# Performance work log

Hardware: AMD Instinct MI355X
Metric: run time of the kernel (lower is better)

The kernel has to match this reference:

```python
import jax, jax.numpy as jnp
import numpy as np

N_NODES = 100000
NEG_SLOPE = 0.2


def gat_conv(x, edge_src, edge_dst, W, att_src, att_dst, bias):
    """PyG-style GATConv with heads=1. edge_src/edge_dst include self-loops.
    x: [N, F_in], W: [F_in, F_out], att_src/att_dst: [F_out], bias: [F_out].
    """
    n = x.shape[0]
    h = x @ W  # [N, F_out]
    a_src = h @ att_src  # [N]
    a_dst = h @ att_dst  # [N]
    e = jax.nn.leaky_relu(a_src[edge_src] + a_dst[edge_dst], NEG_SLOPE)  # [E]
    # segment softmax over edges sharing a destination node
    m = jax.ops.segment_max(e, edge_dst, num_segments=n)  # [N]; self-loops ensure no empty segment
    p = jnp.exp(e - m[edge_dst])
    denom = jax.ops.segment_sum(p, edge_dst, num_segments=n)  # [N]
    alpha = p / denom[edge_dst]  # [E]
    out = jax.ops.segment_sum(alpha[:, None] * h[edge_src], edge_dst, num_segments=n)
    return out + bias


def setup_inputs() -> dict:
    key = jax.random.key(0)
    ks = jax.random.split(key, 16)
    n, e = N_NODES, 1_600_000
    f_in, f_hid, f_out = 128, 64, 32
    x = jax.random.normal(ks[0], (n, f_in), dtype=jnp.float32)
    edge_index = jax.random.randint(ks[1], (2, e), 0, n, dtype=jnp.int32)

    def lin(k, fi, fo):
        return jax.random.normal(k, (fi, fo), dtype=jnp.float32) / np.sqrt(fi).astype(np.float32)

    def att(k, fo):
        return jax.random.normal(k, (fo,), dtype=jnp.float32) / np.sqrt(fo).astype(np.float32)

    return {
        "x": x, "edge_index": edge_index,
        "W1": lin(ks[2], f_in, f_hid), "as1": att(ks[3], f_hid), "ad1": att(ks[4], f_hid),
        "b1": jnp.zeros((f_hid,), jnp.float32),
        "W2": lin(ks[5], f_hid, f_hid), "as2": att(ks[6], f_hid), "ad2": att(ks[7], f_hid),
        "b2": jnp.zeros((f_hid,), jnp.float32),
        "W3": lin(ks[8], f_hid, f_out), "as3": att(ks[9], f_out), "ad3": att(ks[10], f_out),
        "b3": jnp.zeros((f_out,), jnp.float32),
    }


def reference(x, edge_index, W1, as1, ad1, b1, W2, as2, ad2, b2, W3, as3, ad3, b3):
    n = x.shape[0]
    # PyG GATConv default add_self_loops=True
    loops = jnp.arange(n, dtype=edge_index.dtype)
    src = jnp.concatenate([edge_index[0], loops])
    dst = jnp.concatenate([edge_index[1], loops])

    h1 = jax.nn.relu(gat_conv(x, src, dst, W1, as1, ad1, b1))
    h2 = jax.nn.relu(gat_conv(h1, src, dst, W2, as2, ad2, b2))
    out = gat_conv(h2, src, dst, W3, as3, ad3, b3)
    return (out, h1, h2)
```

## Files before the change

### kernel.cpp

```cpp
#include <hip/hip_runtime.h>
#include <hip/hip_bf16.h>

#define NEG_SLOPE 0.2f

__device__ __forceinline__ unsigned short bf16bits(float f) {
    __hip_bfloat16 t = __float2bfloat16(f);
    return *reinterpret_cast<unsigned short*>(&t);
}

template <int FIN, int FOUT>
__global__ __launch_bounds__(256) void node_linear(
    const float* __restrict__ x, const float* __restrict__ W,
    const float* __restrict__ att_s, const float* __restrict__ att_d,
    __hip_bfloat16* __restrict__ h, float* __restrict__ a_s, float* __restrict__ a_d, int n)
{
    constexpr int FG = FOUT / 4;
    constexpr int NG = 256 / FG;
    constexpr int NB = NG * 4;
    constexpr int RS = FIN + 4;
    __shared__ float xs[NB * RS];

    const int tid = threadIdx.x;
    const int base = blockIdx.x * NB;

    constexpr int CNT = NB * FIN / 4 / 256;
    #pragma unroll
    for (int i = 0; i < CNT; ++i) {
        int f4 = tid + 256 * i;
        int node = f4 / (FIN / 4);
        int kk = f4 % (FIN / 4);
        float4 v = make_float4(0.f, 0.f, 0.f, 0.f);
        if (base + node < n) v = *(const float4*)(x + (size_t)(base + node) * FIN + kk * 4);
        *(float4*)(xs + node * RS + kk * 4) = v;
    }
    __syncthreads();

    const int fg = tid % FG;
    const int ng = tid / FG;
    const float* wp = W + fg * 4;
    const float* xr0 = xs + (ng * 4 + 0) * RS;
    const float* xr1 = xs + (ng * 4 + 1) * RS;
    const float* xr2 = xs + (ng * 4 + 2) * RS;
    const float* xr3 = xs + (ng * 4 + 3) * RS;

    float a00=0,a01=0,a02=0,a03=0, a10=0,a11=0,a12=0,a13=0;
    float a20=0,a21=0,a22=0,a23=0, a30=0,a31=0,a32=0,a33=0;
    #pragma unroll 4
    for (int k = 0; k < FIN; ++k) {
        float4 w = *(const float4*)(wp + (size_t)k * FOUT);
        float x0 = xr0[k], x1 = xr1[k], x2 = xr2[k], x3 = xr3[k];
        a00 = fmaf(x0, w.x, a00); a01 = fmaf(x0, w.y, a01);
        a02 = fmaf(x0, w.z, a02); a03 = fmaf(x0, w.w, a03);
        a10 = fmaf(x1, w.x, a10); a11 = fmaf(x1, w.y, a11);
        a12 = fmaf(x1, w.z, a12); a13 = fmaf(x1, w.w, a13);
        a20 = fmaf(x2, w.x, a20); a21 = fmaf(x2, w.y, a21);
        a22 = fmaf(x2, w.z, a22); a23 = fmaf(x2, w.w, a23);
        a30 = fmaf(x3, w.x, a30); a31 = fmaf(x3, w.y, a31);
        a32 = fmaf(x3, w.z, a32); a33 = fmaf(x3, w.w, a33);
    }

    const float4 ats = *(const float4*)(att_s + fg * 4);
    const float4 atd = *(const float4*)(att_d + fg * 4);
    float acc[4][4] = {{a00,a01,a02,a03},{a10,a11,a12,a13},
                       {a20,a21,a22,a23},{a30,a31,a32,a33}};
    #pragma unroll
    for (int i = 0; i < 4; ++i) {
        int node = base + ng * 4 + i;
        float ps = acc[i][0]*ats.x + acc[i][1]*ats.y + acc[i][2]*ats.z + acc[i][3]*ats.w;
        float pd = acc[i][0]*atd.x + acc[i][1]*atd.y + acc[i][2]*atd.z + acc[i][3]*atd.w;
        #pragma unroll
        for (int o = FG / 2; o > 0; o >>= 1) {
            ps += __shfl_xor(ps, o);
            pd += __shfl_xor(pd, o);
        }
        if (fg == 0 && node < n) { a_s[node] = ps; a_d[node] = pd; }
        if (node < n) {
            unsigned w0 = (unsigned)bf16bits(acc[i][0]) | ((unsigned)bf16bits(acc[i][1]) << 16);
            unsigned w1 = (unsigned)bf16bits(acc[i][2]) | ((unsigned)bf16bits(acc[i][3]) << 16);
            uint2 pk; pk.x = w0; pk.y = w1;
            *reinterpret_cast<uint2*>(h + (size_t)node * FOUT + fg * 4) = pk;
        }
    }
}


__global__ __launch_bounds__(256) void sb_hist(
    const int* __restrict__ edst, int E, int n, int* __restrict__ sbhist)
{
    __shared__ int lh[256];
    const int tid = threadIdx.x;
    lh[tid] = 0;
    __syncthreads();
    const int Etot = E + n;
    const int stride = gridDim.x * 256;
    for (int i = blockIdx.x * 256 + tid; i < Etot; i += stride) {
        int d = (i < E) ? edst[i] : i - E;
        atomicAdd(&lh[d >> 9], 1);
    }
    __syncthreads();
    if (lh[tid] > 0) atomicAdd(&sbhist[tid], lh[tid]);
}

__global__ __launch_bounds__(256) void sb_scan(
    const int* __restrict__ sbhist, int nsb, int Etot,
    int* __restrict__ sbbase, int* __restrict__ sbcur)
{
    __shared__ int buf[256];
    const int tid = threadIdx.x;
    int v = (tid < nsb) ? sbhist[tid] : 0;
    buf[tid] = v;
    __syncthreads();
    for (int off = 1; off < 256; off <<= 1) {
        int t = (tid >= off) ? buf[tid - off] : 0;
        __syncthreads();
        buf[tid] += t;
        __syncthreads();
    }
    if (tid < nsb) {
        int ex = buf[tid] - v;
        sbbase[tid] = ex;
        sbcur[tid] = ex;
    }
    if (tid == 0) sbbase[nsb] = Etot;
}

#define CB_CHUNK 4096
#define CB_NSB_MAX 256
__global__ __launch_bounds__(256) void chunk_bin(
    const int* __restrict__ esrc, const int* __restrict__ edst, int E, int n,
    int nsb, int* __restrict__ sbcur, int* __restrict__ packed1)
{
    __shared__ int pk[CB_CHUNK];
    __shared__ unsigned short sbv[CB_CHUNK];
    __shared__ int hist[CB_NSB_MAX];
    __shared__ int gbase[CB_NSB_MAX];
    const int tid = threadIdx.x;
    const int i0 = blockIdx.x * CB_CHUNK;
    const int Etot = E + n;

    hist[tid] = 0;
    __syncthreads();

    for (int j = tid; j < CB_CHUNK; j += 256) {
        int i = i0 + j;
        if (i < Etot) {
            int s, d;
            if (i < E) { s = esrc[i]; d = edst[i]; }
            else       { s = d = i - E; }
            int sb = d >> 9;
            pk[j] = ((d & 511) << 17) | s;
            sbv[j] = (unsigned short)sb;
            atomicAdd(&hist[sb], 1);
        } else {
            sbv[j] = 0xFFFFu;
        }
    }
    __syncthreads();

    if (tid < nsb && hist[tid] > 0)
        gbase[tid] = atomicAdd(&sbcur[tid], hist[tid]);
    hist[tid] = 0;
    __syncthreads();

    for (int j = tid; j < CB_CHUNK; j += 256) {
        unsigned short sb = sbv[j];
        if (sb != 0xFFFFu) {
            int pos = gbase[sb] + atomicAdd(&hist[sb], 1);
            packed1[pos] = pk[j];
        }
    }
}

__global__ __launch_bounds__(256) void sb_sort2(
    const int* __restrict__ sbbase, const int* __restrict__ packed1,
    int* __restrict__ col, int* __restrict__ row_end, int n)
{
    const int sb = blockIdx.x;
    const int node0 = sb << 9;
    const int lo = sbbase[sb];
    const int hi = sbbase[sb + 1];
    const int tid = threadIdx.x;
    __shared__ int c[512];
    __shared__ int sc[512];
    c[tid] = 0; c[tid + 256] = 0;
    __syncthreads();
    for (int j = lo + tid; j < hi; j += 256)
        atomicAdd(&c[((unsigned)packed1[j]) >> 17], 1);
    __syncthreads();
    sc[tid] = c[tid]; sc[tid + 256] = c[tid + 256];
    __syncthreads();
    for (int off = 1; off < 512; off <<= 1) {
        int i0 = tid, i1 = tid + 256;
        int v0 = (i0 >= off) ? sc[i0 - off] : 0;
        int v1 = (i1 >= off) ? sc[i1 - off] : 0;
        __syncthreads();
        sc[i0] += v0; sc[i1] += v1;
        __syncthreads();
    }
    #pragma unroll
    for (int q = 0; q < 2; ++q) {
        int i = tid + q * 256;
        int node = node0 + i;
        if (node < n) row_end[node] = lo + sc[i];
        c[i] = lo + sc[i] - c[i];
    }
    __syncthreads();
    for (int j = lo + tid; j < hi; j += 256) {
        int p = packed1[j];
        int ld = ((unsigned)p) >> 17;
        int pos = atomicAdd(&c[ld], 1);
        col[pos] = p & 0x1FFFF;
    }
}

template <int FOUT>
__global__ __launch_bounds__(256) void gat_aggregate(
    const int* __restrict__ row_end, const int* __restrict__ col,
    const float* __restrict__ a_s, const float* __restrict__ a_d,
    const __hip_bfloat16* __restrict__ h, const float* __restrict__ bias,
    float* __restrict__ outp, int n, int do_relu)
{
    constexpr int NPW = 64 / FOUT;
    const int gwave = (blockIdx.x * 256 + threadIdx.x) >> 6;
    const int lane = threadIdx.x & 63;
    const int node = gwave * NPW + lane / FOUT;
    const int f = lane % FOUT;
    if (node >= n) return;
    const int end = row_end[node];
    const int start = (node == 0) ? 0 : row_end[node - 1];
    const float adn = a_d[node];
    const int egrp = (FOUT == 64) ? 0 : (lane & 32);
    float acc = 0.f, den = 0.f;
    for (int j = start; j < end; j += 8) {
        int k_idx = j + (lane & 7);
        int clamped = (k_idx < end) ? k_idx : (end - 1);
        int sown = col[clamped];
        float eown = a_s[sown] + adn;
        eown = (eown > 0.f) ? eown : NEG_SLOPE * eown;
        float pown = (k_idx < end) ? __expf(eown) : 0.f;
        #pragma unroll
        for (int k = 0; k < 8; ++k) {
            int  sk = __shfl(sown, egrp + k);
            float pk = __shfl(pown, egrp + k);
            den += pk;
            acc = fmaf(pk, __bfloat162float(h[(size_t)sk * FOUT + f]), acc);
        }
    }
    float v = acc / den + bias[f];
    if (do_relu) v = fmaxf(v, 0.f);
    outp[(size_t)node * FOUT + f] = v;
}

extern "C" void kernel_launch(void* const* d_in, const int* in_sizes, int n_in,
                              void* d_out, int out_size, void* d_ws, size_t ws_size,
                              hipStream_t stream)
{
    const float* x   = (const float*)d_in[0];
    const int* eidx  = (const int*)d_in[1];
    const float* W1  = (const float*)d_in[2];
    const float* as1 = (const float*)d_in[3];
    const float* ad1 = (const float*)d_in[4];
    const float* b1  = (const float*)d_in[5];
    const float* W2  = (const float*)d_in[6];
    const float* as2 = (const float*)d_in[7];
    const float* ad2 = (const float*)d_in[8];
    const float* b2  = (const float*)d_in[9];
    const float* W3  = (const float*)d_in[10];
    const float* as3 = (const float*)d_in[11];
    const float* ad3 = (const float*)d_in[12];
    const float* b3  = (const float*)d_in[13];

    const int fhid = in_sizes[3];
    const int fin  = in_sizes[2] / fhid;
    const int fo3  = in_sizes[11];
    const int n    = in_sizes[0] / fin;
    const int E    = in_sizes[1] / 2;
    const int Etot = E + n;
    const int nsb  = (n + 511) >> 9;

    const int* esrc = eidx;
    const int* edst = eidx + E;

    float* out = (float*)d_out;
    float* h1  = out + (size_t)n * fo3;
    float* h2  = h1 + (size_t)n * fhid;

    int* sbhist   = (int*)d_ws;
    int* sbbase   = sbhist + 256;
    int* sbcur    = sbbase + 260;
    int* row_end  = sbcur + 256;
    int* packed1  = row_end + n;
    int* col      = packed1 + Etot;
    __hip_bfloat16* h = (__hip_bfloat16*)(col + Etot);
    float* a_s    = (float*)(h + (size_t)n * fhid);
    float* a_d    = a_s + n;

    const int nchunks = (Etot + CB_CHUNK - 1) / CB_CHUNK;

    hipMemsetAsync(sbhist, 0, 256 * 4, stream);
    sb_hist<<<1024, 256, 0, stream>>>(edst, E, n, sbhist);
    sb_scan<<<1, 256, 0, stream>>>(sbhist, nsb, Etot, sbbase, sbcur);
    chunk_bin<<<nchunks, 256, 0, stream>>>(esrc, edst, E, n, nsb, sbcur, packed1);
    sb_sort2<<<nsb, 256, 0, stream>>>(sbbase, packed1, col, row_end, n);

    const int NLB64  = (n + 63) / 64;
    const int NLB128 = (n + 127) / 128;
    const int AGG64 = (n + 3) / 4;
    const int AGG32 = (n + 7) / 8;

    node_linear<128, 64><<<NLB64, 256, 0, stream>>>(x, W1, as1, ad1, h, a_s, a_d, n);
    gat_aggregate<64><<<AGG64, 256, 0, stream>>>(row_end, col, a_s, a_d, h, b1, h1, n, 1);

    node_linear<64, 64><<<NLB64, 256, 0, stream>>>(h1, W2, as2, ad2, h, a_s, a_d, n);
    gat_aggregate<64><<<AGG64, 256, 0, stream>>>(row_end, col, a_s, a_d, h, b2, h2, n, 1);

    node_linear<64, 32><<<NLB128, 256, 0, stream>>>(h2, W3, as3, ad3, h, a_s, a_d, n);
    gat_aggregate<32><<<AGG32, 256, 0, stream>>>(row_end, col, a_s, a_d, h, b3, out, n, 0);
}
```

Before: 323.9 us.

## Vectorize GAT aggregation to four features per lane, packing more nodes per wave

Each lane in the aggregation kernel now handles four features, read as one 8-byte bf16 load per neighbour and converted with bit shifts. A wave therefore covers four (F=64) or eight (F=32) destination nodes instead of one or two, and the grid sizes shrink to match. The per-chunk neighbour count now equals lanes-per-node with a dynamic trip count, so padded iterations are skipped. The aim is fewer memory instructions and better lane use on low-degree nodes, at the cost of more divergence across nodes with different degrees in one wave.

```diff
diff --git a/kernel.cpp b/kernel.cpp
--- a/kernel.cpp
+++ b/kernel.cpp
@@ -217,38 +217,52 @@
 __global__ __launch_bounds__(256) void gat_aggregate(
     const int* __restrict__ row_end, const int* __restrict__ col,
     const float* __restrict__ a_s, const float* __restrict__ a_d,
-    const __hip_bfloat16* __restrict__ h, const float* __restrict__ bias,
+    const __hip_bfloat16* __restrict__ h_, const float* __restrict__ bias,
     float* __restrict__ outp, int n, int do_relu)
 {
-    constexpr int NPW = 64 / FOUT;
+    constexpr int LPN = FOUT / 4;
+    constexpr int NPW = 64 / LPN;
+    const unsigned short* h = (const unsigned short*)h_;
     const int gwave = (blockIdx.x * 256 + threadIdx.x) >> 6;
     const int lane = threadIdx.x & 63;
-    const int node = gwave * NPW + lane / FOUT;
-    const int f = lane % FOUT;
+    const int node = gwave * NPW + lane / LPN;
+    const int lsub = lane % LPN;
     if (node >= n) return;
     const int end = row_end[node];
     const int start = (node == 0) ? 0 : row_end[node - 1];
     const float adn = a_d[node];
-    const int egrp = (FOUT == 64) ? 0 : (lane & 32);
-    float acc = 0.f, den = 0.f;
-    for (int j = start; j < end; j += 8) {
-        int k_idx = j + (lane & 7);
-        int clamped = (k_idx < end) ? k_idx : (end - 1);
-        int sown = col[clamped];
+    const int egrp = lane & ~(LPN - 1);
+    float acc0 = 0.f, acc1 = 0.f, acc2 = 0.f, acc3 = 0.f, den = 0.f;
+    for (int j = start; j < end; j += LPN) {
+        int kmax = end - j; if (kmax > LPN) kmax = LPN;
+        int k_idx = j + lsub;
+        int sown = col[(k_idx < end) ? k_idx : (end - 1)];
         float eown = a_s[sown] + adn;
         eown = (eown > 0.f) ? eown : NEG_SLOPE * eown;
-        float pown = (k_idx < end) ? __expf(eown) : 0.f;
-        #pragma unroll
-        for (int k = 0; k < 8; ++k) {
-            int  sk = __shfl(sown, egrp + k);
+        float pown = (lsub < kmax) ? __expf(eown) : 0.f;
+        for (int k = 0; k < kmax; ++k) {
+            int   sk = __shfl(sown, egrp + k);
             float pk = __shfl(pown, egrp + k);
             den += pk;
-            acc = fmaf(pk, __bfloat162float(h[(size_t)sk * FOUT + f]), acc);
-        }
-    }
-    float v = acc / den + bias[f];
-    if (do_relu) v = fmaxf(v, 0.f);
-    outp[(size_t)node * FOUT + f] = v;
+            uint2 hv = *(const uint2*)(h + (size_t)sk * FOUT + lsub * 4);
+            acc0 = fmaf(pk, __uint_as_float(hv.x << 16), acc0);
+            acc1 = fmaf(pk, __uint_as_float(hv.x & 0xFFFF0000u), acc1);
+            acc2 = fmaf(pk, __uint_as_float(hv.y << 16), acc2);
+            acc3 = fmaf(pk, __uint_as_float(hv.y & 0xFFFF0000u), acc3);
+        }
+    }
+    const float4 b4 = *(const float4*)(bias + lsub * 4);
+    float inv = 1.f / den;
+    float v0 = acc0 * inv + b4.x;
+    float v1 = acc1 * inv + b4.y;
+    float v2 = acc2 * inv + b4.z;
+    float v3 = acc3 * inv + b4.w;
+    if (do_relu) {
+        v0 = fmaxf(v0, 0.f); v1 = fmaxf(v1, 0.f);
+        v2 = fmaxf(v2, 0.f); v3 = fmaxf(v3, 0.f);
+    }
+    float4 o; o.x = v0; o.y = v1; o.z = v2; o.w = v3;
+    *(float4*)(outp + (size_t)node * FOUT + lsub * 4) = o;
 }
 
 extern "C" void kernel_launch(void* const* d_in, const int* in_sizes, int n_in,
@@ -309,11 +323,11 @@
     const int AGG32 = (n + 7) / 8;
 
     node_linear<128, 64><<<NLB64, 256, 0, stream>>>(x, W1, as1, ad1, h, a_s, a_d, n);
-    gat_aggregate<64><<<AGG64, 256, 0, stream>>>(row_end, col, a_s, a_d, h, b1, h1, n, 1);
+    gat_aggregate<64><<<(n + 15) / 16, 256, 0, stream>>>(row_end, col, a_s, a_d, h, b1, h1, n, 1);
 
     node_linear<64, 64><<<NLB64, 256, 0, stream>>>(h1, W2, as2, ad2, h, a_s, a_d, n);
-    gat_aggregate<64><<<AGG64, 256, 0, stream>>>(row_end, col, a_s, a_d, h, b2, h2, n, 1);
+    gat_aggregate<64><<<(n + 15) / 16, 256, 0, stream>>>(row_end, col, a_s, a_d, h, b2, h2, n, 1);
 
     node_linear<64, 32><<<NLB128, 256, 0, stream>>>(h2, W3, as3, ad3, h, a_s, a_d, n);
-    gat_aggregate<32><<<AGG32, 256, 0, stream>>>(row_end, col, a_s, a_d, h, b3, out, n, 0);
-}
+    gat_aggregate<32><<<(n + 31) / 32, 256, 0, stream>>>(row_end, col, a_s, a_d, h, b3, out, n, 0);
+}
```

New measurement: 323.6 us. No clear change (-0.1%).
